# Performance work log

Hardware: AMD Instinct MI355X
Metric: run time of the kernel (lower is better)

The kernel has to match this reference:

```python
import jax, jax.numpy as jnp
import numpy as np

B, N, D, S, H, ITERS = 8, 2048, 256, 8, 256, 3
EPS = 1e-8
LN_EPS = 1e-5
SCALE = D ** -0.5


def _ln(x):
    # normalize over last axis (affine applied separately per slot)
    mu = jnp.mean(x, axis=-1, keepdims=True)
    var = jnp.var(x, axis=-1, keepdims=True)
    return (x - mu) / jnp.sqrt(var + LN_EPS)


def setup_inputs() -> dict:
    key = jax.random.key(0)
    ks = jax.random.split(key, 24)
    w = lambda k, shape, fan_in: jax.random.normal(k, shape, jnp.float32) / np.sqrt(fan_in)
    inp = {
        "inputs": jax.random.normal(ks[0], (B, N, D), jnp.float32),
        "slot_noise": jax.random.normal(ks[1], (B, S, D), jnp.float32),
        "slots_mu": jax.random.normal(ks[2], (1, S, D), jnp.float32),
        "slots_logsigma": 0.01 * jax.random.normal(ks[3], (1, S, D), jnp.float32),
        # per-slot LayerNorm affines [S, D]
        "g_in": jnp.ones((S, D), jnp.float32), "b_in": jnp.zeros((S, D), jnp.float32),
        "g_ns": jnp.ones((S, D), jnp.float32), "b_ns": jnp.zeros((S, D), jnp.float32),
        "g_pf": jnp.ones((S, D), jnp.float32), "b_pf": jnp.zeros((S, D), jnp.float32),
        # per-slot Linear weights [S, out, in] (torch convention)
        "Wq": w(ks[4], (S, D, D), D), "bq": jnp.zeros((S, D), jnp.float32),
        "Wk": w(ks[5], (S, D, D), D), "bk": jnp.zeros((S, D), jnp.float32),
        "Wv": w(ks[6], (S, D, D), D), "bv": jnp.zeros((S, D), jnp.float32),
        # per-slot GRUCell: [S, 3D, D] (gates order r, z, n as in torch)
        "W_ih": w(ks[7], (S, 3 * D, D), D), "b_ih": jnp.zeros((S, 3 * D), jnp.float32),
        "W_hh": w(ks[8], (S, 3 * D, D), D), "b_hh": jnp.zeros((S, 3 * D), jnp.float32),
        # per-slot MLP (dim -> hidden -> dim)
        "W1": w(ks[9], (S, H, D), D), "b1": jnp.zeros((S, H), jnp.float32),
        "W2": w(ks[10], (S, D, H), H), "b2": jnp.zeros((S, D), jnp.float32),
    }
    return inp


def slot_attention_fwd(inputs, slot_noise, slots_mu, slots_logsigma,
                       g_in, b_in, g_ns, b_ns, g_pf, b_pf,
                       Wq, bq, Wk, bk, Wv, bv,
                       W_ih, b_ih, W_hh, b_hh,
                       W1, b1, W2, b2):
    # slots init: mu + sigma * noise  -> [B, S, D]
    slots = slots_mu + jnp.exp(slots_logsigma) * slot_noise

    # per-slot LayerNorm of inputs: normalization is slot-independent, affine is per-slot
    xn = _ln(inputs)  # [B, N, D]
    inputs_n = xn[:, None, :, :] * g_in[None, :, None, :] + b_in[None, :, None, :]  # [B,S,N,D]

    # per-slot k/v projections as one batched GEMM over the slot axis
    k = jnp.einsum('bsnd,sod->bsno', inputs_n, Wk) + bk[None, :, None, :]  # [B,S,N,D]
    v = jnp.einsum('bsnd,sod->bsno', inputs_n, Wv) + bv[None, :, None, :]

    attn_ori = None
    for _ in range(ITERS):
        slots_prev = slots
        sn = _ln(slots) * g_ns[None] + b_ns[None]                     # [B,S,D]
        q = jnp.einsum('bsd,sod->bso', sn, Wq) + bq[None]             # [B,S,D]
        dots = jnp.einsum('bsd,bsnd->bsn', q, k) * SCALE              # [B,S,N]
        attn_ori = jax.nn.softmax(dots, axis=1) + EPS                 # softmax over slots
        attn = attn_ori / jnp.sum(attn_ori, axis=-1, keepdims=True)   # renormalize over n
        updates = jnp.einsum('bsnd,bsn->bsd', v, attn)                # [B,S,D]

        # per-slot GRUCell: h' = (1-z)*n + z*h
        gi = jnp.einsum('bsd,sod->bso', updates, W_ih) + b_ih[None]   # [B,S,3D]
        gh = jnp.einsum('bsd,sod->bso', slots_prev, W_hh) + b_hh[None]
        gi_r, gi_z, gi_n = jnp.split(gi, 3, axis=-1)
        gh_r, gh_z, gh_n = jnp.split(gh, 3, axis=-1)
        r = jax.nn.sigmoid(gi_r + gh_r)
        z = jax.nn.sigmoid(gi_z + gh_z)
        nn_ = jnp.tanh(gi_n + r * gh_n)
        slots = (1.0 - z) * nn_ + z * slots_prev

        # per-slot MLP residual
        pre = _ln(slots) * g_pf[None] + b_pf[None]
        h1 = jax.nn.relu(jnp.einsum('bsd,shd->bsh', pre, W1) + b1[None])
        slots = slots + jnp.einsum('bsh,sdh->bsd', h1, W2) + b2[None]

    return slots, attn_ori


def reference(inputs, slot_noise, slots_mu, slots_logsigma,
              g_in, b_in, g_ns, b_ns, g_pf, b_pf,
              Wq, bq, Wk, bk, Wv, bv,
              W_ih, b_ih, W_hh, b_hh,
              W1, b1, W2, b2):
    return slot_attention_fwd(inputs, slot_noise, slots_mu, slots_logsigma,
                              g_in, b_in, g_ns, b_ns, g_pf, b_pf,
                              Wq, bq, Wk, bk, Wv, bv,
                              W_ih, b_ih, W_hh, b_hh,
                              W1, b1, W2, b2)
```

## Files before the change

kernel.cpp:

```cpp
#include <hip/hip_runtime.h>
#include <hip/hip_bf16.h>


#define BB 8
#define NT 2048
#define DD 256
#define SS 8
#define HH 256

static constexpr float F_EPS   = 1e-8f;
static constexpr float F_LNEPS = 1e-5f;
static constexpr float F_SCALE = 0.0625f;

__device__ __forceinline__ float wredsum(float v) {
#pragma unroll
  for (int m = 32; m > 0; m >>= 1) v += __shfl_xor(v, m, 64);
  return v;
}
__device__ __forceinline__ float sigm(float x) { return 1.f / (1.f + __expf(-x)); }
__device__ __forceinline__ float tanhfast(float x) {
  float ax = fabsf(x);
  float e = __expf(2.f * ax);
  float t = 1.f - 2.f / (e + 1.f);
  return x < 0.f ? -t : t;
}

__global__ __launch_bounds__(256) void k_init(
    const float* __restrict__ Wk, const float* __restrict__ bk,
    const float* __restrict__ Wv, const float* __restrict__ bv,
    const float* __restrict__ b_in, const float* __restrict__ smu,
    const float* __restrict__ slsig, const float* __restrict__ noise,
    float* __restrict__ ck, float* __restrict__ cv, float* __restrict__ slots) {
  int blk = blockIdx.x;
  int t = threadIdx.x;
  if (blk < 32) {
    int s = blk >> 2, oq = blk & 3;
    int wid = t >> 6, lane = t & 63;
    float4 bi = ((const float4*)(b_in + s*DD))[lane];
    for (int r = 0; r < 16; ++r) {
      int o = oq*64 + wid*16 + r;
      float4 wk4 = ((const float4*)(Wk + ((size_t)s*DD + o)*DD))[lane];
      float4 wv4 = ((const float4*)(Wv + ((size_t)s*DD + o)*DD))[lane];
      float pk = wredsum(bi.x*wk4.x + bi.y*wk4.y + bi.z*wk4.z + bi.w*wk4.w);
      float pv = wredsum(bi.x*wv4.x + bi.y*wv4.y + bi.z*wv4.z + bi.w*wv4.w);
      if (lane == 0) {
        ck[s*DD+o] = pk + bk[s*DD+o];
        cv[s*DD+o] = pv + bv[s*DD+o];
      }
    }
  } else {
    int idx = (blk-32)*256 + t;
    int sd = idx & 2047;
    slots[idx] = smu[sd] + __expf(slsig[sd]) * noise[idx];
  }
}

__global__ __launch_bounds__(256) void k_init2(
    const float* __restrict__ Wq, const float* __restrict__ Wk,
    const float* __restrict__ bq, const float* __restrict__ ck,
    const float* __restrict__ g_in,
    float* __restrict__ Pg, float* __restrict__ vq,
    float* __restrict__ qcon, float* __restrict__ c0) {
  int blk = blockIdx.x;
  int t = threadIdx.x;
  if (blk < 512) {
    __shared__ float Ak[32*33], Aq[32*33];
    int s = blk >> 6, tile = blk & 63;
    int td = tile >> 3, te = tile & 7;
    int dl = t >> 5, el = t & 31;
    float acc[4] = {0.f,0.f,0.f,0.f};
    for (int o0 = 0; o0 < DD; o0 += 32) {
      __syncthreads();
      for (int i = t; i < 1024; i += 256) {
        int o = i >> 5, c = i & 31;
        Ak[o*33+c] = Wk[((size_t)s*DD + o0+o)*DD + td*32 + c];
        Aq[o*33+c] = Wq[((size_t)s*DD + o0+o)*DD + te*32 + c];
      }
      __syncthreads();
#pragma unroll 8
      for (int o = 0; o < 32; ++o) {
        float aq = Aq[o*33+el];
#pragma unroll
        for (int j = 0; j < 4; ++j)
          acc[j] += Ak[o*33 + dl*4 + j] * aq;
      }
    }
#pragma unroll
    for (int j = 0; j < 4; ++j) {
      int d = td*32 + dl*4 + j;
      Pg[((size_t)s*DD + d)*DD + te*32 + el] = g_in[s*DD + d] * acc[j];
    }
  } else {
    __shared__ float cvec[DD];
    __shared__ float part2[8*264];
    int idx = blk - 512;
    int s = idx >> 1, which = idx & 1;
    const float* W = which ? Wk : Wq;
    const float* vec = which ? bq : ck;
    cvec[t] = vec[s*DD + t];
    __syncthreads();
    int og = t >> 5, eg = t & 31;
    float acc[8] = {0.f,0.f,0.f,0.f,0.f,0.f,0.f,0.f};
    for (int oi = 0; oi < 32; ++oi) {
      int o = og*32 + oi;
      float cv2 = cvec[o];
      const float4* wrow = (const float4*)(W + ((size_t)s*DD + o)*DD + eg*8);
      float4 w0 = wrow[0], w1 = wrow[1];
      acc[0] += w0.x*cv2; acc[1] += w0.y*cv2; acc[2] += w0.z*cv2; acc[3] += w0.w*cv2;
      acc[4] += w1.x*cv2; acc[5] += w1.y*cv2; acc[6] += w1.z*cv2; acc[7] += w1.w*cv2;
    }
#pragma unroll
    for (int j = 0; j < 8; ++j) part2[og*264 + eg*8 + j] = acc[j];
    __syncthreads();
    float v = 0.f;
#pragma unroll
    for (int og2 = 0; og2 < 8; ++og2) v += part2[og2*264 + t];
    if (which) qcon[s*DD + t] = v * g_in[s*DD + t];
    else       vq[s*DD + t]   = v;
    if (which == 0 && t < 64) {
      float4 b4 = ((const float4*)(bq + s*DD))[t];
      float4 c4 = ((const float4*)(ck + s*DD))[t];
      float vv = wredsum(b4.x*c4.x + b4.y*c4.y + b4.z*c4.z + b4.w*c4.w);
      if (t == 0) c0[s] = vv;
    }
  }
}

__device__ __forceinline__ int x2i(int bb, int dd) { return bb*288 + (dd>>5)*36 + (dd&31); }

template <typename F>
__device__ __forceinline__ void gemv32(const float* __restrict__ Wrow0,
                                       const float* __restrict__ X2,
                                       float* __restrict__ part, F emit) {
  int t = threadIdx.x;
  int ol = t >> 3, dg = t & 7;
  const float4* wr = (const float4*)(Wrow0 + (size_t)ol*256 + (size_t)dg*32);
  __syncthreads();
  float acc[8] = {0.f,0.f,0.f,0.f,0.f,0.f,0.f,0.f};
#pragma unroll
  for (int j = 0; j < 8; ++j) {
    float4 w4 = wr[j];
    int xo = dg*36 + 4*j;
#pragma unroll
    for (int bbi = 0; bbi < 8; ++bbi) {
      float4 x4 = *(const float4*)&X2[bbi*288 + xo];
      acc[bbi] = fmaf(w4.x,x4.x, fmaf(w4.y,x4.y, fmaf(w4.z,x4.z, fmaf(w4.w,x4.w, acc[bbi]))));
    }
  }
#pragma unroll
  for (int bbi = 0; bbi < 8; ++bbi) part[(ol*8+bbi)*9 + dg] = acc[bbi];
  __syncthreads();
  int o = t >> 3, bbo = t & 7;
  const float* p = &part[(o*8+bbo)*9];
  float v = ((p[0]+p[1])+(p[2]+p[3]))+((p[4]+p[5])+(p[6]+p[7]));
  emit(o, bbo, v);
}

__global__ __launch_bounds__(256) void k_q2(
    const float* __restrict__ slots, const float* __restrict__ g_ns,
    const float* __restrict__ b_ns, const float* __restrict__ Pg,
    const float* __restrict__ qcon, const float* __restrict__ vq,
    const float* __restrict__ c0,
    float* __restrict__ qg, float* __restrict__ qc,
    float* __restrict__ axun, float* __restrict__ rsum) {
  __shared__ __align__(16) float X2[8*288];
  __shared__ float part[32*8*9];
  int blk = blockIdx.x;
  int s = blk >> 3, rc = blk & 7;
  int t = threadIdx.x;
  int wid = t >> 6, lane = t & 63;
  float4 g4 = ((const float4*)(g_ns + s*DD))[lane];
  float4 p4 = ((const float4*)(b_ns + s*DD))[lane];
#pragma unroll
  for (int half = 0; half < 2; ++half) {
    int bb2 = wid + half*4;
    const float4* src = (const float4*)(slots + (size_t)(bb2*8+s)*DD);
    float4 x = src[lane];
    float sv = wredsum(x.x+x.y+x.z+x.w);
    float sq = wredsum(x.x*x.x + x.y*x.y + x.z*x.z + x.w*x.w);
    float mu = sv*(1.f/DD), var = sq*(1.f/DD)-mu*mu, rs = rsqrtf(var+F_LNEPS);
    int base = bb2*288 + (lane>>3)*36 + (lane&7)*4;
    X2[base]   = (x.x-mu)*rs*g4.x + p4.x;
    X2[base+1] = (x.y-mu)*rs*g4.y + p4.y;
    X2[base+2] = (x.z-mu)*rs*g4.z + p4.z;
    X2[base+3] = (x.w-mu)*rs*g4.w + p4.w;
  }
  if (rc == 0) {
    for (int i = t; i < 2048; i += 256) {
      int bb2 = i >> 8, dd = i & 255;
      axun[(size_t)(bb2*8+s)*DD + dd] = 0.f;
    }
    if (t < 8) rsum[t*8+s] = 0.f;
  }
  __syncthreads();
  if (rc == 0) {
    int b = t >> 5, l32 = t & 31;
    float v = 0.f;
#pragma unroll
    for (int j = 0; j < 8; ++j)
      v += X2[b*288 + j*36 + l32] * vq[s*DD + j*32 + l32];
#pragma unroll
    for (int m = 16; m > 0; m >>= 1) v += __shfl_xor(v, m, 64);
    if (l32 == 0) qc[b*8+s] = v + c0[s];
  }
  gemv32(Pg + ((size_t)s*DD + rc*32)*DD, X2, part, [&](int o,int bb2,float v){
    qg[(size_t)(bb2*8+s)*DD + rc*32 + o] = v + qcon[s*DD + rc*32 + o];
  });
}

__global__ __launch_bounds__(256) void k_dots(
    const float* __restrict__ inputs, const float* __restrict__ qg,
    const float* __restrict__ qc, float* __restrict__ axun,
    float* __restrict__ rsum, float* __restrict__ attn_out, int write_attn) {
  __shared__ __align__(16) float qgl[SS*DD];
  __shared__ __align__(16) float xt[32*260];
  __shared__ float dl[8*33];
  __shared__ float qcl[8];
  __shared__ float rsl[8];
  int t = threadIdx.x;
  int b = blockIdx.x >> 5;
  int chunk = blockIdx.x & 31;
  int wid = t >> 6, lane = t & 63;
  for (int i = t; i < SS*DD; i += 256) qgl[i] = qg[(size_t)b*SS*DD + i];
  if (t < 8) { qcl[t] = qc[b*8+t]; rsl[t] = 0.f; }
  int si = t >> 5, ni = t & 31;
  float axa[8] = {0.f,0.f,0.f,0.f,0.f,0.f,0.f,0.f};
  for (int tile = 0; tile < 2; ++tile) {
    int n0 = (chunk*2 + tile) * 32;
    __syncthreads();
#pragma unroll
    for (int rr = 0; rr < 8; ++rr) {
      int r = wid*8 + rr;
      const float4* src = (const float4*)(inputs + ((size_t)b*NT + n0 + r)*DD);
      float4 x = src[lane];
      float sv = wredsum(x.x + x.y + x.z + x.w);
      float sq = wredsum(x.x*x.x + x.y*x.y + x.z*x.z + x.w*x.w);
      float mu = sv*(1.f/DD), var = sq*(1.f/DD)-mu*mu, rs = rsqrtf(var+F_LNEPS);
      float4 o;
      o.x=(x.x-mu)*rs; o.y=(x.y-mu)*rs; o.z=(x.z-mu)*rs; o.w=(x.w-mu)*rs;
      *(float4*)&xt[r*260 + lane*4] = o;
    }
    __syncthreads();
    float acc = 0.f;
    {
      const float4* xr = (const float4*)&xt[ni*260];
      const float4* qr = (const float4*)&qgl[si*DD];
#pragma unroll 8
      for (int j = 0; j < 64; ++j) {
        float4 a4 = xr[j]; float4 b4 = qr[j];
        acc += a4.x*b4.x + a4.y*b4.y + a4.z*b4.z + a4.w*b4.w;
      }
    }
    float dot = (acc + qcl[si]) * F_SCALE;
    dl[si*33+ni] = dot;
    __syncthreads();
    float m = dl[ni];
#pragma unroll
    for (int ss2 = 1; ss2 < 8; ++ss2) m = fmaxf(m, dl[ss2*33+ni]);
    float den = 0.f;
#pragma unroll
    for (int ss2 = 0; ss2 < 8; ++ss2) den += __expf(dl[ss2*33+ni] - m);
    float a = __expf(dot - m) / den + F_EPS;
    __syncthreads();
    dl[si*33+ni] = a;
    float rv = a;
#pragma unroll
    for (int mm = 16; mm > 0; mm >>= 1) rv += __shfl_xor(rv, mm, 64);
    if (ni == 0) rsl[si] += rv;
    if (write_attn) attn_out[(size_t)(b*8+si)*NT + n0 + ni] = a;
    __syncthreads();
#pragma unroll
    for (int n = 0; n < 32; ++n) {
      float x = xt[n*260 + t];
#pragma unroll
      for (int ss2 = 0; ss2 < 8; ++ss2) axa[ss2] += dl[ss2*33+n] * x;
    }
  }
#pragma unroll
  for (int ss2 = 0; ss2 < 8; ++ss2)
    atomicAdd(&axun[(size_t)(b*8+ss2)*DD + t], axa[ss2]);
  __syncthreads();
  if (t < 8) atomicAdd(&rsum[b*8+t], rsl[t]);
}

__global__ __launch_bounds__(256) void k_upd_gh(
    const float* __restrict__ axun, const float* __restrict__ rsum,
    const float* __restrict__ g_in, const float* __restrict__ Wv,
    const float* __restrict__ cv, const float* __restrict__ Whh,
    const float* __restrict__ bhh, const float* __restrict__ slots,
    float* __restrict__ upd, float* __restrict__ ghb) {
  __shared__ __align__(16) float X2[8*288];
  __shared__ float part[32*8*9];
  int blk = blockIdx.x;
  int s = blk >> 5, rc = blk & 31;
  int t = threadIdx.x;
  if (rc < 8) {
    for (int i = t; i < 2048; i += 256) {
      int bb2 = i >> 8, dd = i & 255;
      X2[x2i(bb2,dd)] = axun[(size_t)(bb2*8+s)*DD + dd] / rsum[bb2*8+s] * g_in[s*DD+dd];
    }
    int ob = rc*32;
    gemv32(Wv + ((size_t)s*DD + ob)*DD, X2, part, [&](int o,int bb2,float v){
      upd[(size_t)(bb2*8+s)*DD + ob + o] = v + cv[s*DD + ob + o];
    });
  } else {
    for (int i = t; i < 2048; i += 256) {
      int bb2 = i >> 8, dd = i & 255;
      X2[x2i(bb2,dd)] = slots[(size_t)(bb2*8+s)*DD + dd];
    }
    int ob = (rc-8)*32;
    gemv32(Whh + ((size_t)s*768 + ob)*DD, X2, part, [&](int o,int bb2,float v){
      ghb[(size_t)(bb2*8+s)*768 + ob + o] = v + bhh[s*768 + ob + o];
    });
  }
}

__global__ __launch_bounds__(256) void k_gru(
    const float* __restrict__ upd, const float* __restrict__ Wih,
    const float* __restrict__ bih, const float* __restrict__ ghb,
    const float* __restrict__ slots, float* __restrict__ smid) {
  __shared__ __align__(16) float X2[8*288];
  __shared__ float part[32*8*9];
  int blk = blockIdx.x;
  int s = blk >> 3, jc = blk & 7;
  int t = threadIdx.x;
  for (int i = t; i < 2048; i += 256) {
    int bb2 = i >> 8, dd = i & 255;
    X2[x2i(bb2,dd)] = upd[(size_t)(bb2*8+s)*DD + dd];
  }
  int jb = jc*32;
  float gir = 0.f, giz = 0.f, gin = 0.f;
  gemv32(Wih + ((size_t)s*768 + jb)*DD, X2, part,
         [&](int o,int bb2,float v){ (void)o; (void)bb2; gir = v + bih[s*768 + jb + (threadIdx.x>>3)]; });
  gemv32(Wih + ((size_t)s*768 + 256 + jb)*DD, X2, part,
         [&](int o,int bb2,float v){ (void)o; (void)bb2; giz = v + bih[s*768 + 256 + jb + (threadIdx.x>>3)]; });
  gemv32(Wih + ((size_t)s*768 + 512 + jb)*DD, X2, part,
         [&](int o,int bb2,float v){ (void)o; (void)bb2; gin = v + bih[s*768 + 512 + jb + (threadIdx.x>>3)]; });
  int j = t >> 3, bb2 = t & 7;
  size_t gb = (size_t)(bb2*8+s)*768 + jb + j;
  float r = sigm(gir + ghb[gb]);
  float z = sigm(giz + ghb[gb+256]);
  float nn2 = tanhfast(gin + r*ghb[gb+512]);
  size_t si2 = (size_t)(bb2*8+s)*DD + jb + j;
  float sp = slots[si2];
  smid[si2] = (1.f - z)*nn2 + z*sp;
}

__global__ __launch_bounds__(256) void k_mlp1(
    const float* __restrict__ smid, const float* __restrict__ g_pf,
    const float* __restrict__ b_pf, const float* __restrict__ W1,
    const float* __restrict__ b1, float* __restrict__ h1b) {
  __shared__ __align__(16) float X2[8*288];
  __shared__ float part[32*8*9];
  int blk = blockIdx.x;
  int s = blk >> 3, rc = blk & 7;
  int t = threadIdx.x;
  int wid = t >> 6, lane = t & 63;
#pragma unroll
  for (int half = 0; half < 2; ++half) {
    int bb2 = wid + half*4;
    const float4* src = (const float4*)(smid + (size_t)(bb2*8+s)*DD);
    float4 x = src[lane];
    float sv = wredsum(x.x+x.y+x.z+x.w);
    float sq = wredsum(x.x*x.x + x.y*x.y + x.z*x.z + x.w*x.w);
    float mu = sv*(1.f/DD), var = sq*(1.f/DD)-mu*mu, rs = rsqrtf(var+F_LNEPS);
    float4 g4 = ((const float4*)(g_pf + s*DD))[lane];
    float4 p4 = ((const float4*)(b_pf + s*DD))[lane];
    int base = bb2*288 + (lane>>3)*36 + (lane&7)*4;
    X2[base]   = (x.x-mu)*rs*g4.x + p4.x;
    X2[base+1] = (x.y-mu)*rs*g4.y + p4.y;
    X2[base+2] = (x.z-mu)*rs*g4.z + p4.z;
    X2[base+3] = (x.w-mu)*rs*g4.w + p4.w;
  }
  gemv32(W1 + ((size_t)s*HH + rc*32)*DD, X2, part, [&](int o,int bb2,float v){
    float rr = v + b1[s*HH + rc*32 + o];
    h1b[(size_t)(bb2*8+s)*HH + rc*32 + o] = fmaxf(rr, 0.f);
  });
}

__global__ __launch_bounds__(256) void k_mlp2(
    const float* __restrict__ h1b, const float* __restrict__ W2,
    const float* __restrict__ b2, const float* __restrict__ smid,
    float* __restrict__ slots, float* __restrict__ out_slots, int last) {
  __shared__ __align__(16) float X2[8*288];
  __shared__ float part[32*8*9];
  int blk = blockIdx.x;
  int s = blk >> 3, rc = blk & 7;
  int t = threadIdx.x;
  for (int i = t; i < 2048; i += 256) {
    int bb2 = i >> 8, dd = i & 255;
    X2[x2i(bb2,dd)] = h1b[(size_t)(bb2*8+s)*HH + dd];
  }
  gemv32(W2 + ((size_t)s*DD + rc*32)*HH, X2, part, [&](int o,int bb2,float v){
    int d = rc*32 + o;
    size_t idx = (size_t)(bb2*8+s)*DD + d;
    float rr = v + b2[s*DD + d] + smid[idx];
    slots[idx] = rr;
    if (last) out_slots[idx] = rr;
  });
}

extern "C" void kernel_launch(void* const* d_in, const int* in_sizes, int n_in,
                              void* d_out, int out_size, void* d_ws, size_t ws_size,
                              hipStream_t stream) {
  (void)in_sizes; (void)n_in; (void)out_size; (void)ws_size;
  const float* inputs = (const float*)d_in[0];
  const float* noise  = (const float*)d_in[1];
  const float* smu    = (const float*)d_in[2];
  const float* slsig  = (const float*)d_in[3];
  const float* g_in   = (const float*)d_in[4];
  const float* b_in   = (const float*)d_in[5];
  const float* g_ns   = (const float*)d_in[6];
  const float* b_ns   = (const float*)d_in[7];
  const float* g_pf   = (const float*)d_in[8];
  const float* b_pf   = (const float*)d_in[9];
  const float* Wq  = (const float*)d_in[10];
  const float* bq  = (const float*)d_in[11];
  const float* Wk  = (const float*)d_in[12];
  const float* bk  = (const float*)d_in[13];
  const float* Wv  = (const float*)d_in[14];
  const float* bv  = (const float*)d_in[15];
  const float* Wih = (const float*)d_in[16];
  const float* bih = (const float*)d_in[17];
  const float* Whh = (const float*)d_in[18];
  const float* bhh = (const float*)d_in[19];
  const float* W1  = (const float*)d_in[20];
  const float* b1  = (const float*)d_in[21];
  const float* W2  = (const float*)d_in[22];
  const float* b2  = (const float*)d_in[23];

  float* ws = (float*)d_ws;
  float* slots  = ws;
  float* smid   = slots + BB*SS*DD;
  float* ck     = smid + BB*SS*DD;
  float* cv     = ck + SS*DD;
  float* qg     = cv + SS*DD;
  float* qc     = qg + BB*SS*DD;
  float* rsum   = qc + BB*SS;
  float* axun   = rsum + BB*SS;
  float* upd    = axun + BB*SS*DD;
  float* ghb    = upd + BB*SS*DD;
  float* h1b    = ghb + (size_t)BB*SS*768;
  float* vq     = h1b + BB*SS*HH;
  float* qcon   = vq + SS*DD;
  float* c0     = qcon + SS*DD;
  float* Pg     = c0 + 64;

  float* out_slots = (float*)d_out;
  float* out_attn  = out_slots + BB*SS*DD;

  k_init<<<dim3(96), dim3(256), 0, stream>>>(Wk, bk, Wv, bv, b_in, smu, slsig, noise, ck, cv, slots);
  k_init2<<<dim3(528), dim3(256), 0, stream>>>(Wq, Wk, bq, ck, g_in, Pg, vq, qcon, c0);
  for (int it = 0; it < 3; ++it) {
    int last = (it == 2) ? 1 : 0;
    k_q2<<<dim3(64), dim3(256), 0, stream>>>(slots, g_ns, b_ns, Pg, qcon, vq, c0,
                                             qg, qc, axun, rsum);
    k_dots<<<dim3(256), dim3(256), 0, stream>>>(inputs, qg, qc, axun, rsum, out_attn, last);
    k_upd_gh<<<dim3(256), dim3(256), 0, stream>>>(axun, rsum, g_in, Wv, cv, Whh, bhh,
                                                  slots, upd, ghb);
    k_gru<<<dim3(64), dim3(256), 0, stream>>>(upd, Wih, bih, ghb, slots, smid);
    k_mlp1<<<dim3(64), dim3(256), 0, stream>>>(smid, g_pf, b_pf, W1, b1, h1b);
    k_mlp2<<<dim3(64), dim3(256), 0, stream>>>(h1b, W2, b2, smid, slots, out_slots, last);
  }
}
```

Before: 181.9 us.

## Fuse per-iteration slot update chain into one kernel per (batch,slot)

Merges the update, GRU, MLP and next-iteration query projection kernels into a single k_chain kernel. It runs one block per (batch,slot) that does all the GEMVs back to back through shared memory. The atomicAdd accumulation in k_dots is replaced by per-chunk partial buffers that k_chain reduces, and a new k_init3 computes the first query. This cuts per-iteration launches from six to two and removes the atomics and zeroing. In exchange, each block reads every weight row for its slot separately, so each slot's weights are read 8 times (once per batch) instead of once, and parallelism drops to 64 blocks.

```diff
diff --git a/kernel.cpp b/kernel.cpp
--- a/kernel.cpp
+++ b/kernel.cpp
@@ -1,5 +1,4 @@
 #include <hip/hip_runtime.h>
-#include <hip/hip_bf16.h>
 
 
 #define BB 8
@@ -21,9 +20,29 @@
 __device__ __forceinline__ float tanhfast(float x) {
   float ax = fabsf(x);
   float e = __expf(2.f * ax);
-  float t = 1.f - 2.f / (e + 1.f);
-  return x < 0.f ? -t : t;
-}
+  float t2 = 1.f - 2.f / (e + 1.f);
+  return x < 0.f ? -t2 : t2;
+}
+
+template <typename F>
+__device__ __forceinline__ void gemv_tile(const float* __restrict__ Wrow0,
+                                          const float* __restrict__ xp, F emit) {
+  int t = threadIdx.x;
+  int ol = t >> 3, dg = t & 7;
+  const float4* wr = (const float4*)(Wrow0 + (size_t)ol*256 + dg*32);
+  float acc = 0.f;
+#pragma unroll
+  for (int j = 0; j < 8; ++j) {
+    float4 w4 = wr[j];
+    float4 x4 = *(const float4*)&xp[dg*36 + 4*j];
+    acc = fmaf(w4.x,x4.x, fmaf(w4.y,x4.y, fmaf(w4.z,x4.z, fmaf(w4.w,x4.w, acc))));
+  }
+  acc += __shfl_xor(acc, 1, 64);
+  acc += __shfl_xor(acc, 2, 64);
+  acc += __shfl_xor(acc, 4, 64);
+  if ((t & 7) == 0) emit(ol, acc);
+}
+__device__ __forceinline__ int xpi(int d) { return (d>>5)*36 + (d&31); }
 
 __global__ __launch_bounds__(256) void k_init(
     const float* __restrict__ Wk, const float* __restrict__ bk,
@@ -126,92 +145,42 @@
   }
 }
 
-__device__ __forceinline__ int x2i(int bb, int dd) { return bb*288 + (dd>>5)*36 + (dd&31); }
-
-template <typename F>
-__device__ __forceinline__ void gemv32(const float* __restrict__ Wrow0,
-                                       const float* __restrict__ X2,
-                                       float* __restrict__ part, F emit) {
-  int t = threadIdx.x;
-  int ol = t >> 3, dg = t & 7;
-  const float4* wr = (const float4*)(Wrow0 + (size_t)ol*256 + (size_t)dg*32);
-  __syncthreads();
-  float acc[8] = {0.f,0.f,0.f,0.f,0.f,0.f,0.f,0.f};
-#pragma unroll
-  for (int j = 0; j < 8; ++j) {
-    float4 w4 = wr[j];
-    int xo = dg*36 + 4*j;
-#pragma unroll
-    for (int bbi = 0; bbi < 8; ++bbi) {
-      float4 x4 = *(const float4*)&X2[bbi*288 + xo];
-      acc[bbi] = fmaf(w4.x,x4.x, fmaf(w4.y,x4.y, fmaf(w4.z,x4.z, fmaf(w4.w,x4.w, acc[bbi]))));
-    }
-  }
-#pragma unroll
-  for (int bbi = 0; bbi < 8; ++bbi) part[(ol*8+bbi)*9 + dg] = acc[bbi];
-  __syncthreads();
-  int o = t >> 3, bbo = t & 7;
-  const float* p = &part[(o*8+bbo)*9];
-  float v = ((p[0]+p[1])+(p[2]+p[3]))+((p[4]+p[5])+(p[6]+p[7]));
-  emit(o, bbo, v);
-}
-
-__global__ __launch_bounds__(256) void k_q2(
+__global__ __launch_bounds__(256) void k_init3(
     const float* __restrict__ slots, const float* __restrict__ g_ns,
     const float* __restrict__ b_ns, const float* __restrict__ Pg,
     const float* __restrict__ qcon, const float* __restrict__ vq,
     const float* __restrict__ c0,
-    float* __restrict__ qg, float* __restrict__ qc,
-    float* __restrict__ axun, float* __restrict__ rsum) {
-  __shared__ __align__(16) float X2[8*288];
-  __shared__ float part[32*8*9];
-  int blk = blockIdx.x;
-  int s = blk >> 3, rc = blk & 7;
-  int t = threadIdx.x;
-  int wid = t >> 6, lane = t & 63;
-  float4 g4 = ((const float4*)(g_ns + s*DD))[lane];
-  float4 p4 = ((const float4*)(b_ns + s*DD))[lane];
-#pragma unroll
-  for (int half = 0; half < 2; ++half) {
-    int bb2 = wid + half*4;
-    const float4* src = (const float4*)(slots + (size_t)(bb2*8+s)*DD);
-    float4 x = src[lane];
-    float sv = wredsum(x.x+x.y+x.z+x.w);
-    float sq = wredsum(x.x*x.x + x.y*x.y + x.z*x.z + x.w*x.w);
-    float mu = sv*(1.f/DD), var = sq*(1.f/DD)-mu*mu, rs = rsqrtf(var+F_LNEPS);
-    int base = bb2*288 + (lane>>3)*36 + (lane&7)*4;
-    X2[base]   = (x.x-mu)*rs*g4.x + p4.x;
-    X2[base+1] = (x.y-mu)*rs*g4.y + p4.y;
-    X2[base+2] = (x.z-mu)*rs*g4.z + p4.z;
-    X2[base+3] = (x.w-mu)*rs*g4.w + p4.w;
-  }
-  if (rc == 0) {
-    for (int i = t; i < 2048; i += 256) {
-      int bb2 = i >> 8, dd = i & 255;
-      axun[(size_t)(bb2*8+s)*DD + dd] = 0.f;
-    }
-    if (t < 8) rsum[t*8+s] = 0.f;
-  }
-  __syncthreads();
-  if (rc == 0) {
-    int b = t >> 5, l32 = t & 31;
-    float v = 0.f;
-#pragma unroll
-    for (int j = 0; j < 8; ++j)
-      v += X2[b*288 + j*36 + l32] * vq[s*DD + j*32 + l32];
-#pragma unroll
-    for (int m = 16; m > 0; m >>= 1) v += __shfl_xor(v, m, 64);
-    if (l32 == 0) qc[b*8+s] = v + c0[s];
-  }
-  gemv32(Pg + ((size_t)s*DD + rc*32)*DD, X2, part, [&](int o,int bb2,float v){
-    qg[(size_t)(bb2*8+s)*DD + rc*32 + o] = v + qcon[s*DD + rc*32 + o];
-  });
+    float* __restrict__ qg, float* __restrict__ qc) {
+  __shared__ __align__(16) float xp[288];
+  __shared__ float red[9];
+  int bs = blockIdx.x;
+  int s = bs & 7;
+  int t = threadIdx.x, wid = t >> 6, lane = t & 63;
+  float x = slots[(size_t)bs*DD + t];
+  float sv = wredsum(x), sq = wredsum(x*x);
+  if (lane == 0) { red[wid] = sv; red[4+wid] = sq; }
+  __syncthreads();
+  sv = red[0]+red[1]+red[2]+red[3];
+  sq = red[4]+red[5]+red[6]+red[7];
+  float mu = sv*(1.f/DD), var = sq*(1.f/DD)-mu*mu, rs = rsqrtf(var+F_LNEPS);
+  float sn = (x-mu)*rs*g_ns[s*DD+t] + b_ns[s*DD+t];
+  xp[xpi(t)] = sn;
+  __syncthreads();
+  for (int tl = 0; tl < 8; ++tl)
+    gemv_tile(Pg + ((size_t)s*DD + tl*32)*DD, xp, [&](int o, float v){
+      qg[(size_t)bs*DD + tl*32 + o] = v + qcon[s*DD + tl*32 + o];
+    });
+  float qv = wredsum(sn * vq[s*DD + t]);
+  __syncthreads();
+  if (lane == 0) red[wid] = qv;
+  __syncthreads();
+  if (t == 0) qc[bs] = red[0]+red[1]+red[2]+red[3] + c0[s];
 }
 
 __global__ __launch_bounds__(256) void k_dots(
     const float* __restrict__ inputs, const float* __restrict__ qg,
-    const float* __restrict__ qc, float* __restrict__ axun,
-    float* __restrict__ rsum, float* __restrict__ attn_out, int write_attn) {
+    const float* __restrict__ qc, float* __restrict__ axpart,
+    float* __restrict__ rspart, float* __restrict__ attn_out, int write_attn) {
   __shared__ __align__(16) float qgl[SS*DD];
   __shared__ __align__(16) float xt[32*260];
   __shared__ float dl[8*33];
@@ -278,126 +247,128 @@
   }
 #pragma unroll
   for (int ss2 = 0; ss2 < 8; ++ss2)
-    atomicAdd(&axun[(size_t)(b*8+ss2)*DD + t], axa[ss2]);
-  __syncthreads();
-  if (t < 8) atomicAdd(&rsum[b*8+t], rsl[t]);
-}
-
-__global__ __launch_bounds__(256) void k_upd_gh(
-    const float* __restrict__ axun, const float* __restrict__ rsum,
-    const float* __restrict__ g_in, const float* __restrict__ Wv,
-    const float* __restrict__ cv, const float* __restrict__ Whh,
-    const float* __restrict__ bhh, const float* __restrict__ slots,
-    float* __restrict__ upd, float* __restrict__ ghb) {
-  __shared__ __align__(16) float X2[8*288];
-  __shared__ float part[32*8*9];
-  int blk = blockIdx.x;
-  int s = blk >> 5, rc = blk & 31;
-  int t = threadIdx.x;
-  if (rc < 8) {
-    for (int i = t; i < 2048; i += 256) {
-      int bb2 = i >> 8, dd = i & 255;
-      X2[x2i(bb2,dd)] = axun[(size_t)(bb2*8+s)*DD + dd] / rsum[bb2*8+s] * g_in[s*DD+dd];
-    }
-    int ob = rc*32;
-    gemv32(Wv + ((size_t)s*DD + ob)*DD, X2, part, [&](int o,int bb2,float v){
-      upd[(size_t)(bb2*8+s)*DD + ob + o] = v + cv[s*DD + ob + o];
-    });
-  } else {
-    for (int i = t; i < 2048; i += 256) {
-      int bb2 = i >> 8, dd = i & 255;
-      X2[x2i(bb2,dd)] = slots[(size_t)(bb2*8+s)*DD + dd];
-    }
-    int ob = (rc-8)*32;
-    gemv32(Whh + ((size_t)s*768 + ob)*DD, X2, part, [&](int o,int bb2,float v){
-      ghb[(size_t)(bb2*8+s)*768 + ob + o] = v + bhh[s*768 + ob + o];
-    });
-  }
-}
-
-__global__ __launch_bounds__(256) void k_gru(
-    const float* __restrict__ upd, const float* __restrict__ Wih,
-    const float* __restrict__ bih, const float* __restrict__ ghb,
-    const float* __restrict__ slots, float* __restrict__ smid) {
-  __shared__ __align__(16) float X2[8*288];
-  __shared__ float part[32*8*9];
-  int blk = blockIdx.x;
-  int s = blk >> 3, jc = blk & 7;
-  int t = threadIdx.x;
-  for (int i = t; i < 2048; i += 256) {
-    int bb2 = i >> 8, dd = i & 255;
-    X2[x2i(bb2,dd)] = upd[(size_t)(bb2*8+s)*DD + dd];
-  }
-  int jb = jc*32;
-  float gir = 0.f, giz = 0.f, gin = 0.f;
-  gemv32(Wih + ((size_t)s*768 + jb)*DD, X2, part,
-         [&](int o,int bb2,float v){ (void)o; (void)bb2; gir = v + bih[s*768 + jb + (threadIdx.x>>3)]; });
-  gemv32(Wih + ((size_t)s*768 + 256 + jb)*DD, X2, part,
-         [&](int o,int bb2,float v){ (void)o; (void)bb2; giz = v + bih[s*768 + 256 + jb + (threadIdx.x>>3)]; });
-  gemv32(Wih + ((size_t)s*768 + 512 + jb)*DD, X2, part,
-         [&](int o,int bb2,float v){ (void)o; (void)bb2; gin = v + bih[s*768 + 512 + jb + (threadIdx.x>>3)]; });
-  int j = t >> 3, bb2 = t & 7;
-  size_t gb = (size_t)(bb2*8+s)*768 + jb + j;
-  float r = sigm(gir + ghb[gb]);
-  float z = sigm(giz + ghb[gb+256]);
-  float nn2 = tanhfast(gin + r*ghb[gb+512]);
-  size_t si2 = (size_t)(bb2*8+s)*DD + jb + j;
-  float sp = slots[si2];
-  smid[si2] = (1.f - z)*nn2 + z*sp;
-}
-
-__global__ __launch_bounds__(256) void k_mlp1(
-    const float* __restrict__ smid, const float* __restrict__ g_pf,
-    const float* __restrict__ b_pf, const float* __restrict__ W1,
-    const float* __restrict__ b1, float* __restrict__ h1b) {
-  __shared__ __align__(16) float X2[8*288];
-  __shared__ float part[32*8*9];
-  int blk = blockIdx.x;
-  int s = blk >> 3, rc = blk & 7;
-  int t = threadIdx.x;
-  int wid = t >> 6, lane = t & 63;
-#pragma unroll
-  for (int half = 0; half < 2; ++half) {
-    int bb2 = wid + half*4;
-    const float4* src = (const float4*)(smid + (size_t)(bb2*8+s)*DD);
-    float4 x = src[lane];
-    float sv = wredsum(x.x+x.y+x.z+x.w);
-    float sq = wredsum(x.x*x.x + x.y*x.y + x.z*x.z + x.w*x.w);
-    float mu = sv*(1.f/DD), var = sq*(1.f/DD)-mu*mu, rs = rsqrtf(var+F_LNEPS);
-    float4 g4 = ((const float4*)(g_pf + s*DD))[lane];
-    float4 p4 = ((const float4*)(b_pf + s*DD))[lane];
-    int base = bb2*288 + (lane>>3)*36 + (lane&7)*4;
-    X2[base]   = (x.x-mu)*rs*g4.x + p4.x;
-    X2[base+1] = (x.y-mu)*rs*g4.y + p4.y;
-    X2[base+2] = (x.z-mu)*rs*g4.z + p4.z;
-    X2[base+3] = (x.w-mu)*rs*g4.w + p4.w;
-  }
-  gemv32(W1 + ((size_t)s*HH + rc*32)*DD, X2, part, [&](int o,int bb2,float v){
-    float rr = v + b1[s*HH + rc*32 + o];
-    h1b[(size_t)(bb2*8+s)*HH + rc*32 + o] = fmaxf(rr, 0.f);
-  });
-}
-
-__global__ __launch_bounds__(256) void k_mlp2(
-    const float* __restrict__ h1b, const float* __restrict__ W2,
-    const float* __restrict__ b2, const float* __restrict__ smid,
-    float* __restrict__ slots, float* __restrict__ out_slots, int last) {
-  __shared__ __align__(16) float X2[8*288];
-  __shared__ float part[32*8*9];
-  int blk = blockIdx.x;
-  int s = blk >> 3, rc = blk & 7;
-  int t = threadIdx.x;
-  for (int i = t; i < 2048; i += 256) {
-    int bb2 = i >> 8, dd = i & 255;
-    X2[x2i(bb2,dd)] = h1b[(size_t)(bb2*8+s)*HH + dd];
-  }
-  gemv32(W2 + ((size_t)s*DD + rc*32)*HH, X2, part, [&](int o,int bb2,float v){
-    int d = rc*32 + o;
-    size_t idx = (size_t)(bb2*8+s)*DD + d;
-    float rr = v + b2[s*DD + d] + smid[idx];
-    slots[idx] = rr;
-    if (last) out_slots[idx] = rr;
-  });
+    axpart[((size_t)chunk*64 + b*8 + ss2)*DD + t] = axa[ss2];
+  __syncthreads();
+  if (t < 8) rspart[chunk*64 + b*8 + t] = rsl[t];
+}
+
+__global__ __launch_bounds__(256) void k_chain(
+    float* __restrict__ slots, const float* __restrict__ axpart,
+    const float* __restrict__ rspart, const float* __restrict__ g_in,
+    const float* __restrict__ Wv, const float* __restrict__ cv,
+    const float* __restrict__ Whh, const float* __restrict__ bhh,
+    const float* __restrict__ Wih, const float* __restrict__ bih,
+    const float* __restrict__ g_pf, const float* __restrict__ b_pf,
+    const float* __restrict__ W1, const float* __restrict__ b1,
+    const float* __restrict__ W2, const float* __restrict__ b2,
+    const float* __restrict__ g_ns, const float* __restrict__ b_ns,
+    const float* __restrict__ Pg, const float* __restrict__ qcon,
+    const float* __restrict__ vq, const float* __restrict__ c0,
+    float* __restrict__ qg, float* __restrict__ qc,
+    float* __restrict__ out_slots, int last) {
+  __shared__ __align__(16) float xp[288];
+  __shared__ float ghl[768];
+  __shared__ float gil[768];
+  __shared__ float smidl[DD];
+  __shared__ float bufl[DD];
+  __shared__ float newsl[DD];
+  __shared__ float red[9];
+  int bs = blockIdx.x;
+  int s = bs & 7;
+  int t = threadIdx.x, wid = t >> 6, lane = t & 63;
+
+  float slv = slots[(size_t)bs*DD + t];
+  if (t < 32) {
+    float rv = rspart[t*64 + bs];
+    rv += __shfl_xor(rv, 1, 64);
+    rv += __shfl_xor(rv, 2, 64);
+    rv += __shfl_xor(rv, 4, 64);
+    rv += __shfl_xor(rv, 8, 64);
+    rv += __shfl_xor(rv, 16, 64);
+    if (t == 0) red[8] = rv;
+  }
+  float axv = 0.f;
+#pragma unroll 8
+  for (int c = 0; c < 32; ++c) axv += axpart[((size_t)c*64 + bs)*DD + t];
+
+  xp[xpi(t)] = slv;
+  __syncthreads();
+  for (int tl = 0; tl < 24; ++tl)
+    gemv_tile(Whh + ((size_t)s*768 + tl*32)*DD, xp, [&](int o, float v){
+      ghl[tl*32+o] = v + bhh[s*768 + tl*32 + o]; });
+  __syncthreads();
+
+  float xv = axv / red[8] * g_in[s*DD + t];
+  xp[xpi(t)] = xv;
+  __syncthreads();
+  for (int tl = 0; tl < 8; ++tl)
+    gemv_tile(Wv + ((size_t)s*DD + tl*32)*DD, xp, [&](int o, float v){
+      bufl[tl*32+o] = v + cv[s*DD + tl*32 + o]; });
+  __syncthreads();
+
+  float updv = bufl[t];
+  xp[xpi(t)] = updv;
+  __syncthreads();
+  for (int tl = 0; tl < 24; ++tl)
+    gemv_tile(Wih + ((size_t)s*768 + tl*32)*DD, xp, [&](int o, float v){
+      gil[tl*32+o] = v + bih[s*768 + tl*32 + o]; });
+  __syncthreads();
+
+  float r = sigm(gil[t] + ghl[t]);
+  float z = sigm(gil[256+t] + ghl[256+t]);
+  float nn2 = tanhfast(gil[512+t] + r*ghl[512+t]);
+  float sm = (1.f - z)*nn2 + z*slv;
+  smidl[t] = sm;
+
+  float sv = wredsum(sm), sq = wredsum(sm*sm);
+  if (lane == 0) { red[wid] = sv; red[4+wid] = sq; }
+  __syncthreads();
+  sv = red[0]+red[1]+red[2]+red[3];
+  sq = red[4]+red[5]+red[6]+red[7];
+  float mu = sv*(1.f/DD), var = sq*(1.f/DD)-mu*mu, rs = rsqrtf(var+F_LNEPS);
+  float pre = (sm-mu)*rs*g_pf[s*DD+t] + b_pf[s*DD+t];
+  __syncthreads();
+  xp[xpi(t)] = pre;
+  __syncthreads();
+  for (int tl = 0; tl < 8; ++tl)
+    gemv_tile(W1 + ((size_t)s*HH + tl*32)*DD, xp, [&](int o, float v){
+      bufl[tl*32+o] = fmaxf(v + b1[s*HH + tl*32 + o], 0.f); });
+  __syncthreads();
+
+  float h1v = bufl[t];
+  xp[xpi(t)] = h1v;
+  __syncthreads();
+  for (int tl = 0; tl < 8; ++tl)
+    gemv_tile(W2 + ((size_t)s*DD + tl*32)*HH, xp, [&](int o, float v){
+      int d = tl*32 + o;
+      float out = v + b2[s*DD + d] + smidl[d];
+      size_t gidx = (size_t)bs*DD + d;
+      slots[gidx] = out;
+      if (last) out_slots[gidx] = out;
+      newsl[d] = out; });
+  __syncthreads();
+
+  if (!last) {
+    float nv = newsl[t];
+    float sv2 = wredsum(nv), sq2 = wredsum(nv*nv);
+    if (lane == 0) { red[wid] = sv2; red[4+wid] = sq2; }
+    __syncthreads();
+    sv2 = red[0]+red[1]+red[2]+red[3];
+    sq2 = red[4]+red[5]+red[6]+red[7];
+    float mu2 = sv2*(1.f/DD), var2 = sq2*(1.f/DD)-mu2*mu2, rs2 = rsqrtf(var2+F_LNEPS);
+    float sn = (nv-mu2)*rs2*g_ns[s*DD+t] + b_ns[s*DD+t];
+    __syncthreads();
+    xp[xpi(t)] = sn;
+    __syncthreads();
+    for (int tl = 0; tl < 8; ++tl)
+      gemv_tile(Pg + ((size_t)s*DD + tl*32)*DD, xp, [&](int o, float v){
+        qg[(size_t)bs*DD + tl*32 + o] = v + qcon[s*DD + tl*32 + o]; });
+    float qv = wredsum(sn * vq[s*DD + t]);
+    __syncthreads();
+    if (lane == 0) red[wid] = qv;
+    __syncthreads();
+    if (t == 0) qc[bs] = red[0]+red[1]+red[2]+red[3] + c0[s];
+  }
 }
 
 extern "C" void kernel_launch(void* const* d_in, const int* in_sizes, int n_in,
@@ -430,36 +401,33 @@
   const float* b2  = (const float*)d_in[23];
 
   float* ws = (float*)d_ws;
-  float* slots  = ws;
-  float* smid   = slots + BB*SS*DD;
-  float* ck     = smid + BB*SS*DD;
-  float* cv     = ck + SS*DD;
-  float* qg     = cv + SS*DD;
-  float* qc     = qg + BB*SS*DD;
-  float* rsum   = qc + BB*SS;
-  float* axun   = rsum + BB*SS;
-  float* upd    = axun + BB*SS*DD;
-  float* ghb    = upd + BB*SS*DD;
-  float* h1b    = ghb + (size_t)BB*SS*768;
-  float* vq     = h1b + BB*SS*HH;
-  float* qcon   = vq + SS*DD;
-  float* c0     = qcon + SS*DD;
-  float* Pg     = c0 + 64;
+  float* slots  = ws;                 ws += BB*SS*DD;
+  float* ck     = ws;                 ws += SS*DD;
+  float* cv     = ws;                 ws += SS*DD;
+  float* qg     = ws;                 ws += BB*SS*DD;
+  float* qc     = ws;                 ws += 64;
+  float* axpart = ws;                 ws += 32*64*DD;
+  float* rspart = ws;                 ws += 32*64;
+  float* vq     = ws;                 ws += SS*DD;
+  float* qcon   = ws;                 ws += SS*DD;
+  float* c0     = ws;                 ws += 64;
+  float* Pg     = ws;                 ws += SS*DD*DD;
 
   float* out_slots = (float*)d_out;
   float* out_attn  = out_slots + BB*SS*DD;
 
-  k_init<<<dim3(96), dim3(256), 0, stream>>>(Wk, bk, Wv, bv, b_in, smu, slsig, noise, ck, cv, slots);
+  k_init<<<dim3(96), dim3(256), 0, stream>>>(Wk, bk, Wv, bv, b_in, smu, slsig, noise,
+                                             ck, cv, slots);
   k_init2<<<dim3(528), dim3(256), 0, stream>>>(Wq, Wk, bq, ck, g_in, Pg, vq, qcon, c0);
+  k_init3<<<dim3(64), dim3(256), 0, stream>>>(slots, g_ns, b_ns, Pg, qcon, vq, c0, qg, qc);
   for (int it = 0; it < 3; ++it) {
     int last = (it == 2) ? 1 : 0;
-    k_q2<<<dim3(64), dim3(256), 0, stream>>>(slots, g_ns, b_ns, Pg, qcon, vq, c0,
-                                             qg, qc, axun, rsum);
-    k_dots<<<dim3(256), dim3(256), 0, stream>>>(inputs, qg, qc, axun, rsum, out_attn, last);
-    k_upd_gh<<<dim3(256), dim3(256), 0, stream>>>(axun, rsum, g_in, Wv, cv, Whh, bhh,
-                                                  slots, upd, ghb);
-    k_gru<<<dim3(64), dim3(256), 0, stream>>>(upd, Wih, bih, ghb, slots, smid);
-    k_mlp1<<<dim3(64), dim3(256), 0, stream>>>(smid, g_pf, b_pf, W1, b1, h1b);
-    k_mlp2<<<dim3(64), dim3(256), 0, stream>>>(h1b, W2, b2, smid, slots, out_slots, last);
-  }
-}
+    k_dots<<<dim3(256), dim3(256), 0, stream>>>(inputs, qg, qc, axpart, rspart,
+                                                out_attn, last);
+    k_chain<<<dim3(64), dim3(256), 0, stream>>>(slots, axpart, rspart, g_in,
+                                                Wv, cv, Whh, bhh, Wih, bih,
+                                                g_pf, b_pf, W1, b1, W2, b2,
+                                                g_ns, b_ns, Pg, qcon, vq, c0,
+                                                qg, qc, out_slots, last);
+  }
+}
```

Measured after the change: 375.8 us. +106.6%, slower.

## Precompute W_ih·W_v product and fuse update and GRU gate GEMVs into one kernel

Applied to the files above, without the earlier changes.

The value projection is folded algebraically into the GRU input weights. Wiv = W_ih·W_v and ci = W_ih·cv + b_ih are computed once in a new init kernel, so the per-iteration updates GEMV and its intermediate buffer go away. The hidden-state and input gate GEMVs then run concurrently in a single 512-thread kernel with the gate math fused in, removing one launch per iteration and the global round-trips for ghb and upd. The cost is an extra 1728-block weight-weight matmul at init, about 6 MB of extra workspace, and a small change in rounding order.

```diff
diff --git a/kernel.cpp b/kernel.cpp
--- a/kernel.cpp
+++ b/kernel.cpp
@@ -1,5 +1,4 @@
 #include <hip/hip_runtime.h>
-#include <hip/hip_bf16.h>
 
 
 #define BB 8
@@ -21,8 +20,84 @@
 __device__ __forceinline__ float tanhfast(float x) {
   float ax = fabsf(x);
   float e = __expf(2.f * ax);
-  float t = 1.f - 2.f / (e + 1.f);
-  return x < 0.f ? -t : t;
+  float t2 = 1.f - 2.f / (e + 1.f);
+  return x < 0.f ? -t2 : t2;
+}
+__device__ __forceinline__ int x2i(int bb, int dd) { return bb*288 + (dd>>5)*36 + (dd&31); }
+__device__ __forceinline__ int xpi(int d) { return (d>>5)*36 + (d&31); }
+
+template <typename F>
+__device__ __forceinline__ void gemv32(const float* __restrict__ Wrow0,
+                                       const float* __restrict__ X2,
+                                       float* __restrict__ part, F emit) {
+  int t = threadIdx.x;
+  int ol = t >> 3, dg = t & 7;
+  const float4* wr = (const float4*)(Wrow0 + (size_t)ol*256 + (size_t)dg*32);
+  __syncthreads();
+  float acc[8] = {0.f,0.f,0.f,0.f,0.f,0.f,0.f,0.f};
+#pragma unroll
+  for (int j = 0; j < 8; ++j) {
+    float4 w4 = wr[j];
+    int xo = dg*36 + 4*j;
+#pragma unroll
+    for (int bbi = 0; bbi < 8; ++bbi) {
+      float4 x4 = *(const float4*)&X2[bbi*288 + xo];
+      acc[bbi] = fmaf(w4.x,x4.x, fmaf(w4.y,x4.y, fmaf(w4.z,x4.z, fmaf(w4.w,x4.w, acc[bbi]))));
+    }
+  }
+#pragma unroll
+  for (int bbi = 0; bbi < 8; ++bbi) part[(ol*8+bbi)*9 + dg] = acc[bbi];
+  __syncthreads();
+  int o = t >> 3, bbo = t & 7;
+  const float* pp = &part[(o*8+bbo)*9];
+  float v = ((pp[0]+pp[1])+(pp[2]+pp[3]))+((pp[4]+pp[5])+(pp[6]+pp[7]));
+  emit(o, bbo, v);
+}
+
+template <typename F>
+__device__ __forceinline__ void gemv32h(const float* __restrict__ Wrow0,
+                                        const float* __restrict__ X2,
+                                        float* __restrict__ part, int tid, F emit) {
+  int ol = tid >> 3, dg = tid & 7;
+  const float4* wr = (const float4*)(Wrow0 + (size_t)ol*256 + (size_t)dg*32);
+  __syncthreads();
+  float acc[8] = {0.f,0.f,0.f,0.f,0.f,0.f,0.f,0.f};
+#pragma unroll
+  for (int j = 0; j < 8; ++j) {
+    float4 w4 = wr[j];
+    int xo = dg*36 + 4*j;
+#pragma unroll
+    for (int bbi = 0; bbi < 8; ++bbi) {
+      float4 x4 = *(const float4*)&X2[bbi*288 + xo];
+      acc[bbi] = fmaf(w4.x,x4.x, fmaf(w4.y,x4.y, fmaf(w4.z,x4.z, fmaf(w4.w,x4.w, acc[bbi]))));
+    }
+  }
+#pragma unroll
+  for (int bbi = 0; bbi < 8; ++bbi) part[(ol*8+bbi)*9 + dg] = acc[bbi];
+  __syncthreads();
+  int o = tid >> 3, bbo = tid & 7;
+  const float* pp = &part[(o*8+bbo)*9];
+  float v = ((pp[0]+pp[1])+(pp[2]+pp[3]))+((pp[4]+pp[5])+(pp[6]+pp[7]));
+  emit(o, bbo, v);
+}
+
+template <typename F>
+__device__ __forceinline__ void gemv_tile(const float* __restrict__ Wrow0,
+                                          const float* __restrict__ xp, F emit) {
+  int t = threadIdx.x;
+  int ol = t >> 3, dg = t & 7;
+  const float4* wr = (const float4*)(Wrow0 + (size_t)ol*256 + dg*32);
+  float acc = 0.f;
+#pragma unroll
+  for (int j = 0; j < 8; ++j) {
+    float4 w4 = wr[j];
+    float4 x4 = *(const float4*)&xp[dg*36 + 4*j];
+    acc = fmaf(w4.x,x4.x, fmaf(w4.y,x4.y, fmaf(w4.z,x4.z, fmaf(w4.w,x4.w, acc))));
+  }
+  acc += __shfl_xor(acc, 1, 64);
+  acc += __shfl_xor(acc, 2, 64);
+  acc += __shfl_xor(acc, 4, 64);
+  if ((t & 7) == 0) emit(ol, acc);
 }
 
 __global__ __launch_bounds__(256) void k_init(
@@ -126,34 +201,51 @@
   }
 }
 
-__device__ __forceinline__ int x2i(int bb, int dd) { return bb*288 + (dd>>5)*36 + (dd&31); }
-
-template <typename F>
-__device__ __forceinline__ void gemv32(const float* __restrict__ Wrow0,
-                                       const float* __restrict__ X2,
-                                       float* __restrict__ part, F emit) {
-  int t = threadIdx.x;
-  int ol = t >> 3, dg = t & 7;
-  const float4* wr = (const float4*)(Wrow0 + (size_t)ol*256 + (size_t)dg*32);
-  __syncthreads();
-  float acc[8] = {0.f,0.f,0.f,0.f,0.f,0.f,0.f,0.f};
-#pragma unroll
-  for (int j = 0; j < 8; ++j) {
-    float4 w4 = wr[j];
-    int xo = dg*36 + 4*j;
-#pragma unroll
-    for (int bbi = 0; bbi < 8; ++bbi) {
-      float4 x4 = *(const float4*)&X2[bbi*288 + xo];
-      acc[bbi] = fmaf(w4.x,x4.x, fmaf(w4.y,x4.y, fmaf(w4.z,x4.z, fmaf(w4.w,x4.w, acc[bbi]))));
-    }
-  }
-#pragma unroll
-  for (int bbi = 0; bbi < 8; ++bbi) part[(ol*8+bbi)*9 + dg] = acc[bbi];
-  __syncthreads();
-  int o = t >> 3, bbo = t & 7;
-  const float* p = &part[(o*8+bbo)*9];
-  float v = ((p[0]+p[1])+(p[2]+p[3]))+((p[4]+p[5])+(p[6]+p[7]));
-  emit(o, bbo, v);
+__global__ __launch_bounds__(256) void k_init2b(
+    const float* __restrict__ Wih, const float* __restrict__ Wv,
+    const float* __restrict__ cv, const float* __restrict__ bih,
+    float* __restrict__ Wiv, float* __restrict__ ci) {
+  __shared__ float sm[2112];
+  int blk = blockIdx.x;
+  int t = threadIdx.x;
+  if (blk < 1536) {
+    float* Aih = sm;
+    float* Bv  = sm + 1056;
+    int s = blk / 192, rem = blk % 192;
+    int tj = rem >> 3, td = rem & 7;
+    int dl = t >> 5, el = t & 31;
+    float acc[4] = {0.f,0.f,0.f,0.f};
+    for (int o0 = 0; o0 < DD; o0 += 32) {
+      __syncthreads();
+      for (int i = t; i < 1024; i += 256) {
+        int r = i >> 5, c = i & 31;
+        Aih[r*33+c] = Wih[((size_t)s*768 + tj*32 + r)*DD + o0 + c];
+        Bv[r*33+c]  = Wv[((size_t)s*DD + o0 + r)*DD + td*32 + c];
+      }
+      __syncthreads();
+#pragma unroll 8
+      for (int o = 0; o < 32; ++o) {
+        float bv2 = Bv[o*33+el];
+#pragma unroll
+        for (int j = 0; j < 4; ++j)
+          acc[j] += Aih[(dl*4+j)*33 + o] * bv2;
+      }
+    }
+#pragma unroll
+    for (int j = 0; j < 4; ++j) {
+      int r = tj*32 + dl*4 + j;
+      Wiv[((size_t)s*768 + r)*DD + td*32 + el] = acc[j];
+    }
+  } else {
+    float* xp = sm;
+    int idx = blk - 1536;
+    int s = idx / 24, jt = idx % 24;
+    xp[xpi(t)] = cv[s*DD + t];
+    __syncthreads();
+    gemv_tile(Wih + ((size_t)s*768 + jt*32)*DD, xp, [&](int o, float v){
+      ci[s*768 + jt*32 + o] = v + bih[s*768 + jt*32 + o];
+    });
+  }
 }
 
 __global__ __launch_bounds__(256) void k_q2(
@@ -283,67 +375,54 @@
   if (t < 8) atomicAdd(&rsum[b*8+t], rsl[t]);
 }
 
-__global__ __launch_bounds__(256) void k_upd_gh(
-    const float* __restrict__ axun, const float* __restrict__ rsum,
-    const float* __restrict__ g_in, const float* __restrict__ Wv,
-    const float* __restrict__ cv, const float* __restrict__ Whh,
-    const float* __restrict__ bhh, const float* __restrict__ slots,
-    float* __restrict__ upd, float* __restrict__ ghb) {
-  __shared__ __align__(16) float X2[8*288];
-  __shared__ float part[32*8*9];
-  int blk = blockIdx.x;
-  int s = blk >> 5, rc = blk & 31;
-  int t = threadIdx.x;
-  if (rc < 8) {
-    for (int i = t; i < 2048; i += 256) {
-      int bb2 = i >> 8, dd = i & 255;
-      X2[x2i(bb2,dd)] = axun[(size_t)(bb2*8+s)*DD + dd] / rsum[bb2*8+s] * g_in[s*DD+dd];
-    }
-    int ob = rc*32;
-    gemv32(Wv + ((size_t)s*DD + ob)*DD, X2, part, [&](int o,int bb2,float v){
-      upd[(size_t)(bb2*8+s)*DD + ob + o] = v + cv[s*DD + ob + o];
+__global__ __launch_bounds__(512) void k_gru2(
+    const float* __restrict__ slots, const float* __restrict__ axun,
+    const float* __restrict__ rsum, const float* __restrict__ g_in,
+    const float* __restrict__ Whh, const float* __restrict__ bhh,
+    const float* __restrict__ Wiv, const float* __restrict__ ci,
+    float* __restrict__ smid) {
+  __shared__ __align__(16) float X2s[8*288];
+  __shared__ __align__(16) float X2v[8*288];
+  __shared__ float partA[32*8*9];
+  __shared__ float partB[32*8*9];
+  __shared__ float ghl[3*256];
+  __shared__ float gil[3*256];
+  int blk = blockIdx.x;
+  int s = blk >> 3, jc = blk & 7, jb = jc*32;
+  int t = threadIdx.x;
+  int half = t >> 8, tid = t & 255;
+  if (half == 0) {
+    for (int i = tid; i < 2048; i += 256) {
+      int b = i >> 8, d = i & 255;
+      X2s[x2i(b,d)] = slots[(size_t)(b*8+s)*DD + d];
+    }
+  } else {
+    for (int i = tid; i < 2048; i += 256) {
+      int b = i >> 8, d = i & 255;
+      X2v[x2i(b,d)] = axun[(size_t)(b*8+s)*DD + d] / rsum[b*8+s] * g_in[s*DD+d];
+    }
+  }
+  for (int g = 0; g < 3; ++g) {
+    const float* W = half ? (Wiv + ((size_t)s*768 + g*256 + jb)*DD)
+                          : (Whh + ((size_t)s*768 + g*256 + jb)*DD);
+    const float* X = half ? X2v : X2s;
+    float* pt = half ? partB : partA;
+    float* out = half ? gil : ghl;
+    const float* bias = half ? ci : bhh;
+    gemv32h(W, X, pt, tid, [&](int o,int b,float v){
+      out[g*256 + o*8 + b] = v + bias[s*768 + g*256 + jb + o];
     });
-  } else {
-    for (int i = t; i < 2048; i += 256) {
-      int bb2 = i >> 8, dd = i & 255;
-      X2[x2i(bb2,dd)] = slots[(size_t)(bb2*8+s)*DD + dd];
-    }
-    int ob = (rc-8)*32;
-    gemv32(Whh + ((size_t)s*768 + ob)*DD, X2, part, [&](int o,int bb2,float v){
-      ghb[(size_t)(bb2*8+s)*768 + ob + o] = v + bhh[s*768 + ob + o];
-    });
-  }
-}
-
-__global__ __launch_bounds__(256) void k_gru(
-    const float* __restrict__ upd, const float* __restrict__ Wih,
-    const float* __restrict__ bih, const float* __restrict__ ghb,
-    const float* __restrict__ slots, float* __restrict__ smid) {
-  __shared__ __align__(16) float X2[8*288];
-  __shared__ float part[32*8*9];
-  int blk = blockIdx.x;
-  int s = blk >> 3, jc = blk & 7;
-  int t = threadIdx.x;
-  for (int i = t; i < 2048; i += 256) {
-    int bb2 = i >> 8, dd = i & 255;
-    X2[x2i(bb2,dd)] = upd[(size_t)(bb2*8+s)*DD + dd];
-  }
-  int jb = jc*32;
-  float gir = 0.f, giz = 0.f, gin = 0.f;
-  gemv32(Wih + ((size_t)s*768 + jb)*DD, X2, part,
-         [&](int o,int bb2,float v){ (void)o; (void)bb2; gir = v + bih[s*768 + jb + (threadIdx.x>>3)]; });
-  gemv32(Wih + ((size_t)s*768 + 256 + jb)*DD, X2, part,
-         [&](int o,int bb2,float v){ (void)o; (void)bb2; giz = v + bih[s*768 + 256 + jb + (threadIdx.x>>3)]; });
-  gemv32(Wih + ((size_t)s*768 + 512 + jb)*DD, X2, part,
-         [&](int o,int bb2,float v){ (void)o; (void)bb2; gin = v + bih[s*768 + 512 + jb + (threadIdx.x>>3)]; });
-  int j = t >> 3, bb2 = t & 7;
-  size_t gb = (size_t)(bb2*8+s)*768 + jb + j;
-  float r = sigm(gir + ghb[gb]);
-  float z = sigm(giz + ghb[gb+256]);
-  float nn2 = tanhfast(gin + r*ghb[gb+512]);
-  size_t si2 = (size_t)(bb2*8+s)*DD + jb + j;
-  float sp = slots[si2];
-  smid[si2] = (1.f - z)*nn2 + z*sp;
+  }
+  __syncthreads();
+  if (half == 0) {
+    int o = tid >> 3, b = tid & 7;
+    int d = jb + o;
+    float hprev = X2s[x2i(b,d)];
+    float r = sigm(gil[o*8+b] + ghl[o*8+b]);
+    float z = sigm(gil[256 + o*8+b] + ghl[256 + o*8+b]);
+    float nn2 = tanhfast(gil[512 + o*8+b] + r*ghl[512 + o*8+b]);
+    smid[(size_t)(b*8+s)*DD + d] = (1.f - z)*nn2 + z*hprev;
+  }
 }
 
 __global__ __launch_bounds__(256) void k_mlp1(
@@ -430,36 +509,42 @@
   const float* b2  = (const float*)d_in[23];
 
   float* ws = (float*)d_ws;
-  float* slots  = ws;
-  float* smid   = slots + BB*SS*DD;
-  float* ck     = smid + BB*SS*DD;
-  float* cv     = ck + SS*DD;
-  float* qg     = cv + SS*DD;
-  float* qc     = qg + BB*SS*DD;
-  float* rsum   = qc + BB*SS;
-  float* axun   = rsum + BB*SS;
-  float* upd    = axun + BB*SS*DD;
-  float* ghb    = upd + BB*SS*DD;
-  float* h1b    = ghb + (size_t)BB*SS*768;
-  float* vq     = h1b + BB*SS*HH;
-  float* qcon   = vq + SS*DD;
-  float* c0     = qcon + SS*DD;
-  float* Pg     = c0 + 64;
+  float* slots  = ws;                 ws += BB*SS*DD;
+  float* smid   = ws;                 ws += BB*SS*DD;
+  float* ck     = ws;                 ws += SS*DD;
+  float* cv     = ws;                 ws += SS*DD;
+  float* qg     = ws;                 ws += BB*SS*DD;
+  float* qc     = ws;                 ws += 64;
+  float* rsum   = ws;                 ws += 64;
+  float* axun   = ws;                 ws += BB*SS*DD;
+  float* h1b    = ws;                 ws += BB*SS*HH;
+  float* vq     = ws;                 ws += SS*DD;
+  float* qcon   = ws;                 ws += SS*DD;
+  float* c0     = ws;                 ws += 64;
+  float* ci     = ws;                 ws += SS*768;
+  float* Pg     = ws;                 ws += (size_t)SS*DD*DD;
+  float* Wiv    = ws;                 ws += (size_t)SS*768*DD;
 
   float* out_slots = (float*)d_out;
   float* out_attn  = out_slots + BB*SS*DD;
 
-  k_init<<<dim3(96), dim3(256), 0, stream>>>(Wk, bk, Wv, bv, b_in, smu, slsig, noise, ck, cv, slots);
+  k_init<<<dim3(96), dim3(256), 0, stream>>>(Wk, bk, Wv, bv, b_in, smu, slsig, noise,
+                                             ck, cv, slots);
   k_init2<<<dim3(528), dim3(256), 0, stream>>>(Wq, Wk, bq, ck, g_in, Pg, vq, qcon, c0);
+  k_init2b<<<dim3(1728), dim3(256), 0, stream>>>(Wih, Wv, cv, bih, Wiv, ci);
+  k_q2<<<dim3(64), dim3(256), 0, stream>>>(slots, g_ns, b_ns, Pg, qcon, vq, c0,
+                                           qg, qc, axun, rsum);
   for (int it = 0; it < 3; ++it) {
     int last = (it == 2) ? 1 : 0;
-    k_q2<<<dim3(64), dim3(256), 0, stream>>>(slots, g_ns, b_ns, Pg, qcon, vq, c0,
-                                             qg, qc, axun, rsum);
-    k_dots<<<dim3(256), dim3(256), 0, stream>>>(inputs, qg, qc, axun, rsum, out_attn, last);
-    k_upd_gh<<<dim3(256), dim3(256), 0, stream>>>(axun, rsum, g_in, Wv, cv, Whh, bhh,
-                                                  slots, upd, ghb);
-    k_gru<<<dim3(64), dim3(256), 0, stream>>>(upd, Wih, bih, ghb, slots, smid);
+    k_dots<<<dim3(256), dim3(256), 0, stream>>>(inputs, qg, qc, axun, rsum,
+                                                out_attn, last);
+    k_gru2<<<dim3(64), dim3(512), 0, stream>>>(slots, axun, rsum, g_in,
+                                               Whh, bhh, Wiv, ci, smid);
     k_mlp1<<<dim3(64), dim3(256), 0, stream>>>(smid, g_pf, b_pf, W1, b1, h1b);
-    k_mlp2<<<dim3(64), dim3(256), 0, stream>>>(h1b, W2, b2, smid, slots, out_slots, last);
-  }
-}
+    k_mlp2<<<dim3(64), dim3(256), 0, stream>>>(h1b, W2, b2, smid, slots,
+                                               out_slots, last);
+    if (!last)
+      k_q2<<<dim3(64), dim3(256), 0, stream>>>(slots, g_ns, b_ns, Pg, qcon, vq, c0,
+                                               qg, qc, axun, rsum);
+  }
+}
```

Measured after the change: 215.7 us. 1.19x slower.
